# Kernel tuning notes

Hardware: AMD Instinct MI355X
Metric: run time of the kernel (lower is better)

## Reference

```python
import jax, jax.numpy as jnp
import numpy as np

N_NODES = 100000
N_EDGES = 1600000
IN_DIM, HID_DIM, OUT_DIM = 128, 128, 47
BN_EPS = 1e-5


def setup_inputs() -> dict:
    key = jax.random.key(0)
    ks = jax.random.split(key, 12)
    x = jax.random.normal(ks[0], (N_NODES, IN_DIM), dtype=jnp.float32)
    edge_index = jax.random.randint(ks[1], (2, N_EDGES), 0, N_NODES, dtype=jnp.int32)
    def glorot(k, fan_in, fan_out):
        s = jnp.sqrt(6.0 / (fan_in + fan_out))
        return jax.random.uniform(k, (fan_in, fan_out), jnp.float32, -s, s)
    return {
        "x": x,
        "edge_index": edge_index,
        "W0": glorot(ks[2], IN_DIM, HID_DIM), "b0": jnp.zeros((HID_DIM,), jnp.float32),
        "W1": glorot(ks[3], HID_DIM, HID_DIM), "b1": jnp.zeros((HID_DIM,), jnp.float32),
        "W2": glorot(ks[4], HID_DIM, OUT_DIM), "b2": jnp.zeros((OUT_DIM,), jnp.float32),
        "g0": jnp.ones((HID_DIM,), jnp.float32), "be0": jnp.zeros((HID_DIM,), jnp.float32),
        "g1": jnp.ones((HID_DIM,), jnp.float32), "be1": jnp.zeros((HID_DIM,), jnp.float32),
    }


def _gcn_norm(edge_index, n_nodes):
    # add self-loops, compute sym-normalized edge weights (PyG GCNConv default)
    loop = jnp.arange(n_nodes, dtype=edge_index.dtype)
    src = jnp.concatenate([edge_index[0], loop])
    dst = jnp.concatenate([edge_index[1], loop])
    deg = jax.ops.segment_sum(jnp.ones_like(dst, dtype=jnp.float32), dst,
                              num_segments=n_nodes)
    dinv = jnp.where(deg > 0, jax.lax.rsqrt(deg), 0.0)
    norm = dinv[src] * dinv[dst]  # [E + N]
    return src, dst, norm


def _conv(x, W, b, src, dst, norm, n_nodes):
    h = x @ W                                   # [N, d_out]
    msg = h[src] * norm[:, None]                # gather + scale
    out = jax.ops.segment_sum(msg, dst, num_segments=n_nodes)
    return out + b


def _batchnorm(h, gamma, beta):
    mean = jnp.mean(h, axis=0)
    var = jnp.mean(jnp.square(h - mean), axis=0)  # biased var (torch BN)
    return (h - mean) * jax.lax.rsqrt(var + BN_EPS) * gamma + beta


def reference(x, edge_index, W0, b0, W1, b1, W2, b2, g0, be0, g1, be1):
    n = x.shape[0]
    src, dst, norm = _gcn_norm(edge_index, n)
    h = _conv(x, W0, b0, src, dst, norm, n)
    h = jax.nn.relu(_batchnorm(h, g0, be0))     # dropout = identity (eval)
    h = _conv(h, W1, b1, src, dst, norm, n)
    h = jax.nn.relu(_batchnorm(h, g1, be1))
    h = _conv(h, W2, b2, src, dst, norm, n)
    return jax.nn.log_softmax(h, axis=-1)
```

## Files before the change

kernel.cpp:

```cpp
#include <hip/hip_runtime.h>
#include <math.h>

#define N_NODES 100000
#define N_EDGES 1600000
#define HID 128
#define OUTD 47
#define OSTR 48

#define NPB 128
#define NB 782
#define BCAP 2560
#define CHUNK 2048
#define NCHB 782
#define CWB 64

typedef short bf16x8 __attribute__((ext_vector_type(8)));
typedef float f32x4 __attribute__((ext_vector_type(4)));

__device__ inline unsigned short f2bf(float x) {
    union { float f; unsigned int u; } v; v.f = x;
    unsigned int r = v.u + 0x7fffu + ((v.u >> 16) & 1u);
    return (unsigned short)(r >> 16);
}
__device__ inline float bf_lo(unsigned int u) { return __uint_as_float(u << 16); }
__device__ inline float bf_hi(unsigned int u) { return __uint_as_float(u & 0xffff0000u); }

__device__ inline unsigned int src_chunk(unsigned int s) {
    return (s * 42950u) >> 28;
}


__global__ __launch_bounds__(256) void binA_k(
    const int* __restrict__ src, const int* __restrict__ dst,
    int* __restrict__ gcur, unsigned int* __restrict__ binned,
    const float* __restrict__ W0, const float* __restrict__ W1, const float* __restrict__ W2,
    unsigned short* __restrict__ Wt0, unsigned short* __restrict__ Wt1,
    unsigned short* __restrict__ Wt2)
{
    __shared__ unsigned int sortedL[CHUNK];
    __shared__ unsigned short bucketOf[CHUNK];
    __shared__ int cntL[NB];
    __shared__ int excL[NB];
    __shared__ int curL[NB];
    __shared__ int gposL[NB];
    __shared__ int partial[256];

    int t = threadIdx.x;

    if (blockIdx.x >= NCHB) {
        int i = (blockIdx.x - NCHB) * 256 + t;
        if (i < 16384) {
            int n = i >> 7, k = i & 127;
            Wt0[i] = f2bf(W0[k * 128 + n]);
            Wt1[i] = f2bf(W1[k * 128 + n]);
        }
        if (i < 48 * 128) {
            int n = i >> 7, k = i & 127;
            Wt2[i] = (n < OUTD) ? f2bf(W2[k * OUTD + n]) : (unsigned short)0;
        }
        return;
    }

    int e0 = blockIdx.x * CHUNK;

    for (int i = t; i < NB; i += 256) cntL[i] = 0;
    __syncthreads();

    for (int i = t; i < CHUNK; i += 256) {
        int e = e0 + i;
        if (e < N_EDGES) atomicAdd(&cntL[dst[e] >> 7], 1);
    }
    __syncthreads();

    int b4 = t * 4;
    int c0 = (b4 + 0 < NB) ? cntL[b4 + 0] : 0;
    int c1 = (b4 + 1 < NB) ? cntL[b4 + 1] : 0;
    int c2 = (b4 + 2 < NB) ? cntL[b4 + 2] : 0;
    int c3 = (b4 + 3 < NB) ? cntL[b4 + 3] : 0;
    int lsum = c0 + c1 + c2 + c3;
    partial[t] = lsum;
    __syncthreads();
    for (int off = 1; off < 256; off <<= 1) {
        int x = (t >= off) ? partial[t - off] : 0;
        __syncthreads();
        partial[t] += x;
        __syncthreads();
    }
    int pbase = partial[t] - lsum;
    if (b4 + 0 < NB) { excL[b4 + 0] = pbase;                curL[b4 + 0] = pbase; }
    if (b4 + 1 < NB) { excL[b4 + 1] = pbase + c0;           curL[b4 + 1] = pbase + c0; }
    if (b4 + 2 < NB) { excL[b4 + 2] = pbase + c0 + c1;      curL[b4 + 2] = pbase + c0 + c1; }
    if (b4 + 3 < NB) { excL[b4 + 3] = pbase + c0 + c1 + c2; curL[b4 + 3] = pbase + c0 + c1 + c2; }
    __syncthreads();

    int tot = partial[255];

    for (int i = t; i < CHUNK; i += 256) {
        int e = e0 + i;
        if (e < N_EDGES) {
            int d = dst[e];
            int s = src[e];
            int bkt = d >> 7;
            int pos = atomicAdd(&curL[bkt], 1);
            sortedL[pos] = ((unsigned int)s << 7) | (unsigned int)(d & 127);
            bucketOf[pos] = (unsigned short)bkt;
        }
    }
    __syncthreads();

    for (int b = t; b < NB; b += 256) {
        int c = cntL[b];
        gposL[b] = c ? atomicAdd(&gcur[b], c) : 0;
    }
    __syncthreads();

    for (int i = t; i < tot; i += 256) {
        unsigned int r = sortedL[i];
        int bkt = bucketOf[i];
        binned[(size_t)bkt * BCAP + gposL[bkt] + (i - excL[bkt])] = r;
    }
}


__global__ __launch_bounds__(256) void binB_k(
    const unsigned int* __restrict__ binned, const int* __restrict__ gcur,
    int2* __restrict__ rowse, float* __restrict__ dinv, int* __restrict__ colv)
{
    __shared__ unsigned int recL[BCAP];
    __shared__ int colL[BCAP];
    __shared__ int hist[2048];
    __shared__ int partial[256];

    int b = blockIdx.x, t = threadIdx.x;
    int cnt = gcur[b];
    int base = b * BCAP;
    const unsigned int* rp = binned + (size_t)b * BCAP;

    for (int i = t; i < 2048; i += 256) hist[i] = 0;
    __syncthreads();

    for (int i = t; i < cnt; i += 256) {
        unsigned int r = rp[i];
        recL[i] = r;
        unsigned int key = ((r & 127u) << 4) | src_chunk(r >> 7);
        atomicAdd(&hist[key], 1);
    }
    __syncthreads();

    int base8 = t * 8;
    int v[8], lsum = 0;
#pragma unroll
    for (int j = 0; j < 8; j++) { v[j] = hist[base8 + j]; lsum += v[j]; }
    partial[t] = lsum;
    __syncthreads();
    for (int off = 1; off < 256; off <<= 1) {
        int x = (t >= off) ? partial[t - off] : 0;
        __syncthreads();
        partial[t] += x;
        __syncthreads();
    }
    int run = partial[t] - lsum;
#pragma unroll
    for (int j = 0; j < 8; j++) { hist[base8 + j] = run; run += v[j]; }
    __syncthreads();

    if (t < NPB) {
        int node = b * NPB + t;
        if (node < N_NODES) {
            int start = hist[t << 4];
            int end = (t < NPB - 1) ? hist[(t + 1) << 4] : cnt;
            rowse[node] = make_int2(base + start, base + end);
            dinv[node] = rsqrtf((float)(end - start + 1));
        }
    }
    __syncthreads();

    for (int i = t; i < cnt; i += 256) {
        unsigned int r = recL[i];
        unsigned int key = ((r & 127u) << 4) | src_chunk(r >> 7);
        int pos = atomicAdd(&hist[key], 1);
        colL[pos] = (int)(r >> 7);
    }
    __syncthreads();
    for (int i = t; i < cnt; i += 256) colv[base + i] = colL[i];
}


template <int ABF16, int MODE, int NT, int OBF16>
__global__ __launch_bounds__(256) void gemm_k(
    const void* __restrict__ Ap, const unsigned short* __restrict__ Wt,
    const float* __restrict__ bnSum, const float* __restrict__ bnSq,
    const float* __restrict__ gam, const float* __restrict__ bet,
    const float* __restrict__ dinv, void* __restrict__ Outp,
    int ncols, int ostride)
{
    __shared__ unsigned short WtL[NT * 16][136];
    __shared__ float sS[128], sT[128];

    int t = threadIdx.x;
    if (MODE) {
        if (t < 128) {
            float mean = bnSum[t] * (1.0f / N_NODES);
            float var = bnSq[t] * (1.0f / N_NODES) - mean * mean;
            float inv = rsqrtf(var + 1e-5f);
            float s = gam[t] * inv;
            sS[t] = s;
            sT[t] = bet[t] - mean * s;
        }
    }

    const int TOT = NT * 16 * 128;
    for (int e = t * 8; e < TOT; e += 256 * 8) {
        int n = e >> 7, k = e & 127;
        uint4 v = *(const uint4*)(Wt + e);
        *(uint4*)&WtL[n][k] = v;
    }
    __syncthreads();

    int wave = t >> 6, lane = t & 63;
    int quad = lane >> 4, m16 = lane & 15;
    int rbase = blockIdx.x * 128 + wave * 32;

    f32x4 acc[2][NT];
#pragma unroll
    for (int rt = 0; rt < 2; rt++)
#pragma unroll
        for (int ct = 0; ct < NT; ct++) acc[rt][ct] = (f32x4){0.f, 0.f, 0.f, 0.f};

#pragma unroll
    for (int kc = 0; kc < 4; kc++) {
        int kb = kc * 32 + quad * 8;
        bf16x8 afrag[2];
#pragma unroll
        for (int rt = 0; rt < 2; rt++) {
            int row = rbase + rt * 16 + m16;
            bool rv = (row < N_NODES);
            if (ABF16) {
                uint4 v = make_uint4(0, 0, 0, 0);
                if (rv) v = *(const uint4*)((const unsigned short*)Ap + (size_t)row * 128 + kb);
                if (MODE) {
                    unsigned int uu[4] = {v.x, v.y, v.z, v.w};
                    unsigned short* fp = (unsigned short*)&afrag[rt];
#pragma unroll
                    for (int i = 0; i < 4; i++) {
                        int k0 = kb + 2 * i;
                        float lo = fmaxf(bf_lo(uu[i]) * sS[k0] + sT[k0], 0.f);
                        float hi = fmaxf(bf_hi(uu[i]) * sS[k0 + 1] + sT[k0 + 1], 0.f);
                        fp[2 * i] = f2bf(lo);
                        fp[2 * i + 1] = f2bf(hi);
                    }
                } else {
                    afrag[rt] = *(bf16x8*)&v;
                }
            } else {
                const float* ap = (const float*)Ap + (size_t)row * 128 + kb;
                float4 f0 = make_float4(0.f, 0.f, 0.f, 0.f), f1 = f0;
                if (rv) { f0 = *(const float4*)ap; f1 = *(const float4*)(ap + 4); }
                unsigned short* fp = (unsigned short*)&afrag[rt];
                fp[0] = f2bf(f0.x); fp[1] = f2bf(f0.y); fp[2] = f2bf(f0.z); fp[3] = f2bf(f0.w);
                fp[4] = f2bf(f1.x); fp[5] = f2bf(f1.y); fp[6] = f2bf(f1.z); fp[7] = f2bf(f1.w);
            }
        }
#pragma unroll
        for (int ct = 0; ct < NT; ct++) {
            bf16x8 bfrag = *(bf16x8*)&WtL[ct * 16 + m16][kb];
#pragma unroll
            for (int rt = 0; rt < 2; rt++)
                acc[rt][ct] = __builtin_amdgcn_mfma_f32_16x16x32_bf16(
                    afrag[rt], bfrag, acc[rt][ct], 0, 0, 0);
        }
    }

#pragma unroll
    for (int rt = 0; rt < 2; rt++)
#pragma unroll
        for (int r = 0; r < 4; r++) {
            int row = rbase + rt * 16 + quad * 4 + r;
            if (row < N_NODES) {
                float d = dinv[row];
#pragma unroll
                for (int ct = 0; ct < NT; ct++) {
                    int c = ct * 16 + m16;
                    if (c < ncols) {
                        float val = acc[rt][ct][r] * d;
                        if (OBF16)
                            ((unsigned short*)Outp)[(size_t)row * ostride + c] = f2bf(val);
                        else
                            ((float*)Outp)[(size_t)row * ostride + c] = val;
                    }
                }
            }
        }
}


__global__ __launch_bounds__(256) void agg_k(
    const unsigned int* __restrict__ H, const int2* __restrict__ rowse,
    const int* __restrict__ colv, const float* __restrict__ dinv,
    const float* __restrict__ bias, unsigned int* __restrict__ out)
{
    int gw = (blockIdx.x * 256 + threadIdx.x) >> 6;
    int lane = threadIdx.x & 63;
    if (gw >= N_NODES) return;
    int q = lane >> 4;
    int c = lane & 15;
    int2 se = rowse[gw];
    int rp = se.x, re = se.y;
    const uint4* H4 = (const uint4*)H;

    float a0 = 0.f, a1 = 0.f, a2 = 0.f, a3 = 0.f;
    float a4 = 0.f, a5 = 0.f, a6 = 0.f, a7 = 0.f;
    if (q == 0) {
        uint4 u = H4[(size_t)gw * 16 + c];
        a0 = bf_lo(u.x); a1 = bf_hi(u.x); a2 = bf_lo(u.y); a3 = bf_hi(u.y);
        a4 = bf_lo(u.z); a5 = bf_hi(u.z); a6 = bf_lo(u.w); a7 = bf_hi(u.w);
    }

    for (int j0 = rp; j0 < re; j0 += 64) {
        int idx = (j0 + lane < re) ? colv[j0 + lane] : 0;
        int n = min(64, re - j0);
        int nq = n >> 2;
        int t4 = 0;
        for (; t4 + 1 < nq; t4 += 2) {
            int sa = __shfl(idx, 4 * t4 + q);
            int sb = __shfl(idx, 4 * t4 + 4 + q);
            uint4 ua = H4[(size_t)sa * 16 + c];
            uint4 ub = H4[(size_t)sb * 16 + c];
            a0 += bf_lo(ua.x) + bf_lo(ub.x);
            a1 += bf_hi(ua.x) + bf_hi(ub.x);
            a2 += bf_lo(ua.y) + bf_lo(ub.y);
            a3 += bf_hi(ua.y) + bf_hi(ub.y);
            a4 += bf_lo(ua.z) + bf_lo(ub.z);
            a5 += bf_hi(ua.z) + bf_hi(ub.z);
            a6 += bf_lo(ua.w) + bf_lo(ub.w);
            a7 += bf_hi(ua.w) + bf_hi(ub.w);
        }
        if (t4 < nq) {
            int sa = __shfl(idx, 4 * t4 + q);
            uint4 ua = H4[(size_t)sa * 16 + c];
            a0 += bf_lo(ua.x); a1 += bf_hi(ua.x);
            a2 += bf_lo(ua.y); a3 += bf_hi(ua.y);
            a4 += bf_lo(ua.z); a5 += bf_hi(ua.z);
            a6 += bf_lo(ua.w); a7 += bf_hi(ua.w);
        }
        int rem = n & 3;
        if (rem) {
            int sa = __shfl(idx, (n - rem) + q);
            if (q < rem) {
                uint4 ua = H4[(size_t)sa * 16 + c];
                a0 += bf_lo(ua.x); a1 += bf_hi(ua.x);
                a2 += bf_lo(ua.y); a3 += bf_hi(ua.y);
                a4 += bf_lo(ua.z); a5 += bf_hi(ua.z);
                a6 += bf_lo(ua.w); a7 += bf_hi(ua.w);
            }
        }
    }

    a0 += __shfl_xor(a0, 16); a0 += __shfl_xor(a0, 32);
    a1 += __shfl_xor(a1, 16); a1 += __shfl_xor(a1, 32);
    a2 += __shfl_xor(a2, 16); a2 += __shfl_xor(a2, 32);
    a3 += __shfl_xor(a3, 16); a3 += __shfl_xor(a3, 32);
    a4 += __shfl_xor(a4, 16); a4 += __shfl_xor(a4, 32);
    a5 += __shfl_xor(a5, 16); a5 += __shfl_xor(a5, 32);
    a6 += __shfl_xor(a6, 16); a6 += __shfl_xor(a6, 32);
    a7 += __shfl_xor(a7, 16); a7 += __shfl_xor(a7, 32);

    if (q == 0) {
        float d = dinv[gw];
        float4 ba = ((const float4*)bias)[2 * c];
        float4 bb = ((const float4*)bias)[2 * c + 1];
        uint4 r;
        r.x = (unsigned int)f2bf(a0 * d + ba.x) | ((unsigned int)f2bf(a1 * d + ba.y) << 16);
        r.y = (unsigned int)f2bf(a2 * d + ba.z) | ((unsigned int)f2bf(a3 * d + ba.w) << 16);
        r.z = (unsigned int)f2bf(a4 * d + bb.x) | ((unsigned int)f2bf(a5 * d + bb.y) << 16);
        r.w = (unsigned int)f2bf(a6 * d + bb.z) | ((unsigned int)f2bf(a7 * d + bb.w) << 16);
        ((uint4*)out)[(size_t)gw * 16 + c] = r;
    }
}


__global__ __launch_bounds__(256) void agg_out_k(
    const unsigned int* __restrict__ H, const int2* __restrict__ rowse,
    const int* __restrict__ colv, const float* __restrict__ dinv,
    const float* __restrict__ b2, float* __restrict__ out)
{
    int gw = (blockIdx.x * 256 + threadIdx.x) >> 6;
    int lane = threadIdx.x & 63;
    if (gw >= N_NODES) return;
    int q = lane >> 4;
    int c = lane & 15;
    bool ld = c < 12;
    int2 se = rowse[gw];
    int rp = se.x, re = se.y;
    const uint2* H2 = (const uint2*)H;

    float a0 = 0.f, a1 = 0.f, a2 = 0.f, a3 = 0.f;
    if (q == 0 && ld) {
        uint2 u = H2[(size_t)gw * 12 + c];
        a0 = bf_lo(u.x); a1 = bf_hi(u.x); a2 = bf_lo(u.y); a3 = bf_hi(u.y);
    }

    for (int j0 = rp; j0 < re; j0 += 64) {
        int idx = (j0 + lane < re) ? colv[j0 + lane] : 0;
        int n = min(64, re - j0);
        int nq = n >> 2;
        int t4 = 0;
        for (; t4 + 1 < nq; t4 += 2) {
            int sa = __shfl(idx, 4 * t4 + q);
            int sb = __shfl(idx, 4 * t4 + 4 + q);
            if (ld) {
                uint2 ua = H2[(size_t)sa * 12 + c];
                uint2 ub = H2[(size_t)sb * 12 + c];
                a0 += bf_lo(ua.x) + bf_lo(ub.x);
                a1 += bf_hi(ua.x) + bf_hi(ub.x);
                a2 += bf_lo(ua.y) + bf_lo(ub.y);
                a3 += bf_hi(ua.y) + bf_hi(ub.y);
            }
        }
        if (t4 < nq) {
            int sa = __shfl(idx, 4 * t4 + q);
            if (ld) {
                uint2 ua = H2[(size_t)sa * 12 + c];
                a0 += bf_lo(ua.x); a1 += bf_hi(ua.x);
                a2 += bf_lo(ua.y); a3 += bf_hi(ua.y);
            }
        }
        int rem = n & 3;
        if (rem) {
            int sa = __shfl(idx, (n - rem) + q);
            if (q < rem && ld) {
                uint2 ua = H2[(size_t)sa * 12 + c];
                a0 += bf_lo(ua.x); a1 += bf_hi(ua.x);
                a2 += bf_lo(ua.y); a3 += bf_hi(ua.y);
            }
        }
    }

    a0 += __shfl_xor(a0, 16); a0 += __shfl_xor(a0, 32);
    a1 += __shfl_xor(a1, 16); a1 += __shfl_xor(a1, 32);
    a2 += __shfl_xor(a2, 16); a2 += __shfl_xor(a2, 32);
    a3 += __shfl_xor(a3, 16); a3 += __shfl_xor(a3, 32);

    float d = dinv[gw];
    int ch = c * 4;
    float v0 = -INFINITY, v1 = -INFINITY, v2 = -INFINITY, v3 = -INFINITY;
    if (ld) {
        v0 = a0 * d + b2[ch];
        v1 = a1 * d + b2[ch + 1];
        v2 = a2 * d + b2[ch + 2];
        if (ch + 3 < OUTD) v3 = a3 * d + b2[ch + 3];
    }
    float m = fmaxf(fmaxf(v0, v1), fmaxf(v2, v3));
    m = fmaxf(m, __shfl_xor(m, 1));
    m = fmaxf(m, __shfl_xor(m, 2));
    m = fmaxf(m, __shfl_xor(m, 4));
    m = fmaxf(m, __shfl_xor(m, 8));
    float e = 0.f;
    if (ld) {
        e = __expf(v0 - m) + __expf(v1 - m) + __expf(v2 - m);
        if (ch + 3 < OUTD) e += __expf(v3 - m);
    }
    float sum = e;
    sum += __shfl_xor(sum, 1);
    sum += __shfl_xor(sum, 2);
    sum += __shfl_xor(sum, 4);
    sum += __shfl_xor(sum, 8);
    float ls = logf(sum);
    if (q == 0 && ld) {
        float* op = out + (size_t)gw * OUTD + ch;
        op[0] = v0 - m - ls;
        op[1] = v1 - m - ls;
        op[2] = v2 - m - ls;
        if (ch + 3 < OUTD) op[3] = v3 - m - ls;
    }
}


__global__ __launch_bounds__(256) void bnstats_k(const unsigned int* __restrict__ H,
                                                 float* __restrict__ sum,
                                                 float* __restrict__ sq)
{
    __shared__ float2 ls[256], lq[256];
    int t = threadIdx.x;
    int idx = blockIdx.x * 256 + t;
    int stride = gridDim.x * 256;
    float sx = 0.f, sy = 0.f, qx = 0.f, qy = 0.f;
    for (; idx < N_NODES * 64; idx += stride) {
        unsigned int u = H[idx];
        float x = bf_lo(u), y = bf_hi(u);
        sx += x; sy += y; qx += x * x; qy += y * y;
    }
    ls[t] = make_float2(sx, sy);
    lq[t] = make_float2(qx, qy);
    __syncthreads();
    if (t < 64) {
        float2 a = ls[t], b = ls[t + 64], c = ls[t + 128], d = ls[t + 192];
        float2 e = lq[t], f = lq[t + 64], g = lq[t + 128], h = lq[t + 192];
        int c0 = t * 2;
        atomicAdd(&sum[c0],     a.x + b.x + c.x + d.x);
        atomicAdd(&sum[c0 + 1], a.y + b.y + c.y + d.y);
        atomicAdd(&sq[c0],      e.x + f.x + g.x + h.x);
        atomicAdd(&sq[c0 + 1],  e.y + f.y + g.y + h.y);
    }
}


extern "C" void kernel_launch(void* const* d_in, const int* in_sizes, int n_in,
                              void* d_out, int out_size, void* d_ws, size_t ws_size,
                              hipStream_t stream)
{
    const float* x   = (const float*)d_in[0];
    const int*   ei  = (const int*)d_in[1];
    const float* W0  = (const float*)d_in[2];
    const float* b0  = (const float*)d_in[3];
    const float* W1  = (const float*)d_in[4];
    const float* b1  = (const float*)d_in[5];
    const float* W2  = (const float*)d_in[6];
    const float* b2  = (const float*)d_in[7];
    const float* g0  = (const float*)d_in[8];
    const float* be0 = (const float*)d_in[9];
    const float* g1  = (const float*)d_in[10];
    const float* be1 = (const float*)d_in[11];
    const int* srcv = ei;
    const int* dstv = ei + N_EDGES;

    char* w = (char*)d_ws;
    unsigned int* H0 = (unsigned int*)w;  w += (size_t)N_NODES * 128 * 2;
    unsigned int* H1 = (unsigned int*)w;  w += (size_t)N_NODES * 128 * 2;
    unsigned int* Hf = (unsigned int*)w;  w += (size_t)N_NODES * OSTR * 2;
    unsigned int* binned = (unsigned int*)w; w += (size_t)NB * BCAP * 4;
    int* colv = (int*)w;        w += (size_t)NB * BCAP * 4;
    unsigned short* Wt0 = (unsigned short*)w; w += 16384 * 2;
    unsigned short* Wt1 = (unsigned short*)w; w += 16384 * 2;
    unsigned short* Wt2 = (unsigned short*)w; w += 48 * 128 * 2;
    int2* rowse = (int2*)w;     w += (size_t)N_NODES * 8;
    float* dinv = (float*)w;    w += (size_t)N_NODES * 4;
    int* gcur = (int*)w;        w += 784 * 4;
    float* bnS0 = (float*)w;    w += 128 * 4;
    float* bnQ0 = (float*)w;    w += 128 * 4;
    float* bnS1 = (float*)w;    w += 128 * 4;
    float* bnQ1 = (float*)w;    w += 128 * 4;

    int gb = (N_NODES + 127) / 128;
    int ab = (N_NODES * 64 + 255) / 256;

    hipMemsetAsync(gcur, 0, (784 + 512) * 4, stream);

    binA_k<<<NCHB + CWB, 256, 0, stream>>>(srcv, dstv, gcur, binned,
                                           W0, W1, W2, Wt0, Wt1, Wt2);
    binB_k<<<NB, 256, 0, stream>>>(binned, gcur, rowse, dinv, colv);

    gemm_k<0, 0, 8, 1><<<gb, 256, 0, stream>>>(x, Wt0, nullptr, nullptr, nullptr, nullptr,
                                               dinv, H0, 128, 128);
    agg_k<<<ab, 256, 0, stream>>>(H0, rowse, colv, dinv, b0, H1);
    bnstats_k<<<512, 256, 0, stream>>>(H1, bnS0, bnQ0);

    gemm_k<1, 1, 8, 1><<<gb, 256, 0, stream>>>(H1, Wt1, bnS0, bnQ0, g0, be0,
                                               dinv, H0, 128, 128);
    agg_k<<<ab, 256, 0, stream>>>(H0, rowse, colv, dinv, b1, H1);
    bnstats_k<<<512, 256, 0, stream>>>(H1, bnS1, bnQ1);

    gemm_k<1, 1, 3, 1><<<gb, 256, 0, stream>>>(H1, Wt2, bnS1, bnQ1, g1, be1,
                                               dinv, Hf, OUTD, OSTR);
    agg_out_k<<<ab, 256, 0, stream>>>(Hf, rowse, colv, dinv, b2, (float*)d_out);
}
```

Before: 474.6 us.

## Fuse batchnorm statistics into aggregation and process four nodes per wavefront

The aggregation kernel now gives each 16-lane quarter of a wavefront its own destination node, instead of splitting one node's edges across the whole wavefront and reducing with cross-lane shuffles. Each quarter loads up to 16 neighbour indices at a time and issues up to eight gathers before accumulating. The separate bnstats kernel is removed: per-channel sum and sum-of-squares are reduced in shared memory across a 1024-thread block and added atomically. This drops two launches and one full re-read of the hidden activations. In exchange, nodes with different degrees in one wavefront cause lane divergence, and statistics are taken from pre-rounding fp32 values rather than the stored bf16 ones.

```diff
diff --git a/kernel.cpp b/kernel.cpp
--- a/kernel.cpp
+++ b/kernel.cpp
@@ -13,6 +13,7 @@
 #define CHUNK 2048
 #define NCHB 782
 #define CWB 64
+#define NAB 1563
 
 typedef short bf16x8 __attribute__((ext_vector_type(8)));
 typedef float f32x4 __attribute__((ext_vector_type(4)));
@@ -294,87 +295,145 @@
 }
 
 
-__global__ __launch_bounds__(256) void agg_k(
+__global__ __launch_bounds__(1024) void agg4_k(
     const unsigned int* __restrict__ H, const int2* __restrict__ rowse,
     const int* __restrict__ colv, const float* __restrict__ dinv,
-    const float* __restrict__ bias, unsigned int* __restrict__ out)
+    const float* __restrict__ bias,
+    float* __restrict__ bnSum, float* __restrict__ bnSq,
+    unsigned int* __restrict__ out)
 {
-    int gw = (blockIdx.x * 256 + threadIdx.x) >> 6;
-    int lane = threadIdx.x & 63;
-    if (gw >= N_NODES) return;
-    int q = lane >> 4;
-    int c = lane & 15;
-    int2 se = rowse[gw];
-    int rp = se.x, re = se.y;
+    __shared__ float red[2][16][16][8];
+
+    int t = threadIdx.x;
+    int w = t >> 6, lane = t & 63;
+    int q = lane >> 4, c = lane & 15;
+    int qb = q << 4;
+    int node = blockIdx.x * 64 + w * 4 + q;
+    bool valid = node < N_NODES;
+
     const uint4* H4 = (const uint4*)H;
 
     float a0 = 0.f, a1 = 0.f, a2 = 0.f, a3 = 0.f;
     float a4 = 0.f, a5 = 0.f, a6 = 0.f, a7 = 0.f;
-    if (q == 0) {
-        uint4 u = H4[(size_t)gw * 16 + c];
+    int rp = 0, re = 0;
+    float dv = 0.f;
+    if (valid) {
+        int2 se = rowse[node];
+        rp = se.x; re = se.y;
+        dv = dinv[node];
+        uint4 u = H4[(size_t)node * 16 + c];
         a0 = bf_lo(u.x); a1 = bf_hi(u.x); a2 = bf_lo(u.y); a3 = bf_hi(u.y);
         a4 = bf_lo(u.z); a5 = bf_hi(u.z); a6 = bf_lo(u.w); a7 = bf_hi(u.w);
     }
 
-    for (int j0 = rp; j0 < re; j0 += 64) {
-        int idx = (j0 + lane < re) ? colv[j0 + lane] : 0;
-        int n = min(64, re - j0);
-        int nq = n >> 2;
-        int t4 = 0;
-        for (; t4 + 1 < nq; t4 += 2) {
-            int sa = __shfl(idx, 4 * t4 + q);
-            int sb = __shfl(idx, 4 * t4 + 4 + q);
-            uint4 ua = H4[(size_t)sa * 16 + c];
-            uint4 ub = H4[(size_t)sb * 16 + c];
-            a0 += bf_lo(ua.x) + bf_lo(ub.x);
-            a1 += bf_hi(ua.x) + bf_hi(ub.x);
-            a2 += bf_lo(ua.y) + bf_lo(ub.y);
-            a3 += bf_hi(ua.y) + bf_hi(ub.y);
-            a4 += bf_lo(ua.z) + bf_lo(ub.z);
-            a5 += bf_hi(ua.z) + bf_hi(ub.z);
-            a6 += bf_lo(ua.w) + bf_lo(ub.w);
-            a7 += bf_hi(ua.w) + bf_hi(ub.w);
-        }
-        if (t4 < nq) {
-            int sa = __shfl(idx, 4 * t4 + q);
-            uint4 ua = H4[(size_t)sa * 16 + c];
-            a0 += bf_lo(ua.x); a1 += bf_hi(ua.x);
-            a2 += bf_lo(ua.y); a3 += bf_hi(ua.y);
-            a4 += bf_lo(ua.z); a5 += bf_hi(ua.z);
-            a6 += bf_lo(ua.w); a7 += bf_hi(ua.w);
-        }
-        int rem = n & 3;
-        if (rem) {
-            int sa = __shfl(idx, (n - rem) + q);
-            if (q < rem) {
-                uint4 ua = H4[(size_t)sa * 16 + c];
-                a0 += bf_lo(ua.x); a1 += bf_hi(ua.x);
-                a2 += bf_lo(ua.y); a3 += bf_hi(ua.y);
-                a4 += bf_lo(ua.z); a5 += bf_hi(ua.z);
-                a6 += bf_lo(ua.w); a7 += bf_hi(ua.w);
-            }
-        }
-    }
-
-    a0 += __shfl_xor(a0, 16); a0 += __shfl_xor(a0, 32);
-    a1 += __shfl_xor(a1, 16); a1 += __shfl_xor(a1, 32);
-    a2 += __shfl_xor(a2, 16); a2 += __shfl_xor(a2, 32);
-    a3 += __shfl_xor(a3, 16); a3 += __shfl_xor(a3, 32);
-    a4 += __shfl_xor(a4, 16); a4 += __shfl_xor(a4, 32);
-    a5 += __shfl_xor(a5, 16); a5 += __shfl_xor(a5, 32);
-    a6 += __shfl_xor(a6, 16); a6 += __shfl_xor(a6, 32);
-    a7 += __shfl_xor(a7, 16); a7 += __shfl_xor(a7, 32);
-
+    for (int j0 = rp; j0 < re; j0 += 16) {
+        int m = min(16, re - j0);
+        int idx = (c < m) ? colv[j0 + c] : 0;
+        int tt = 0;
+        for (; tt + 8 <= m; tt += 8) {
+            int s0 = __shfl(idx, qb + tt + 0);
+            int s1 = __shfl(idx, qb + tt + 1);
+            int s2 = __shfl(idx, qb + tt + 2);
+            int s3 = __shfl(idx, qb + tt + 3);
+            int s4 = __shfl(idx, qb + tt + 4);
+            int s5 = __shfl(idx, qb + tt + 5);
+            int s6 = __shfl(idx, qb + tt + 6);
+            int s7 = __shfl(idx, qb + tt + 7);
+            uint4 u0 = H4[(size_t)s0 * 16 + c];
+            uint4 u1 = H4[(size_t)s1 * 16 + c];
+            uint4 u2 = H4[(size_t)s2 * 16 + c];
+            uint4 u3 = H4[(size_t)s3 * 16 + c];
+            uint4 u4 = H4[(size_t)s4 * 16 + c];
+            uint4 u5 = H4[(size_t)s5 * 16 + c];
+            uint4 u6 = H4[(size_t)s6 * 16 + c];
+            uint4 u7 = H4[(size_t)s7 * 16 + c];
+            a0 += (bf_lo(u0.x) + bf_lo(u1.x)) + (bf_lo(u2.x) + bf_lo(u3.x))
+                + (bf_lo(u4.x) + bf_lo(u5.x)) + (bf_lo(u6.x) + bf_lo(u7.x));
+            a1 += (bf_hi(u0.x) + bf_hi(u1.x)) + (bf_hi(u2.x) + bf_hi(u3.x))
+                + (bf_hi(u4.x) + bf_hi(u5.x)) + (bf_hi(u6.x) + bf_hi(u7.x));
+            a2 += (bf_lo(u0.y) + bf_lo(u1.y)) + (bf_lo(u2.y) + bf_lo(u3.y))
+                + (bf_lo(u4.y) + bf_lo(u5.y)) + (bf_lo(u6.y) + bf_lo(u7.y));
+            a3 += (bf_hi(u0.y) + bf_hi(u1.y)) + (bf_hi(u2.y) + bf_hi(u3.y))
+                + (bf_hi(u4.y) + bf_hi(u5.y)) + (bf_hi(u6.y) + bf_hi(u7.y));
+            a4 += (bf_lo(u0.z) + bf_lo(u1.z)) + (bf_lo(u2.z) + bf_lo(u3.z))
+                + (bf_lo(u4.z) + bf_lo(u5.z)) + (bf_lo(u6.z) + bf_lo(u7.z));
+            a5 += (bf_hi(u0.z) + bf_hi(u1.z)) + (bf_hi(u2.z) + bf_hi(u3.z))
+                + (bf_hi(u4.z) + bf_hi(u5.z)) + (bf_hi(u6.z) + bf_hi(u7.z));
+            a6 += (bf_lo(u0.w) + bf_lo(u1.w)) + (bf_lo(u2.w) + bf_lo(u3.w))
+                + (bf_lo(u4.w) + bf_lo(u5.w)) + (bf_lo(u6.w) + bf_lo(u7.w));
+            a7 += (bf_hi(u0.w) + bf_hi(u1.w)) + (bf_hi(u2.w) + bf_hi(u3.w))
+                + (bf_hi(u4.w) + bf_hi(u5.w)) + (bf_hi(u6.w) + bf_hi(u7.w));
+        }
+        for (; tt + 4 <= m; tt += 4) {
+            int s0 = __shfl(idx, qb + tt + 0);
+            int s1 = __shfl(idx, qb + tt + 1);
+            int s2 = __shfl(idx, qb + tt + 2);
+            int s3 = __shfl(idx, qb + tt + 3);
+            uint4 u0 = H4[(size_t)s0 * 16 + c];
+            uint4 u1 = H4[(size_t)s1 * 16 + c];
+            uint4 u2 = H4[(size_t)s2 * 16 + c];
+            uint4 u3 = H4[(size_t)s3 * 16 + c];
+            a0 += (bf_lo(u0.x) + bf_lo(u1.x)) + (bf_lo(u2.x) + bf_lo(u3.x));
+            a1 += (bf_hi(u0.x) + bf_hi(u1.x)) + (bf_hi(u2.x) + bf_hi(u3.x));
+            a2 += (bf_lo(u0.y) + bf_lo(u1.y)) + (bf_lo(u2.y) + bf_lo(u3.y));
+            a3 += (bf_hi(u0.y) + bf_hi(u1.y)) + (bf_hi(u2.y) + bf_hi(u3.y));
+            a4 += (bf_lo(u0.z) + bf_lo(u1.z)) + (bf_lo(u2.z) + bf_lo(u3.z));
+            a5 += (bf_hi(u0.z) + bf_hi(u1.z)) + (bf_hi(u2.z) + bf_hi(u3.z));
+            a6 += (bf_lo(u0.w) + bf_lo(u1.w)) + (bf_lo(u2.w) + bf_lo(u3.w));
+            a7 += (bf_hi(u0.w) + bf_hi(u1.w)) + (bf_hi(u2.w) + bf_hi(u3.w));
+        }
+        for (; tt < m; tt++) {
+            int s0 = __shfl(idx, qb + tt);
+            uint4 u0 = H4[(size_t)s0 * 16 + c];
+            a0 += bf_lo(u0.x); a1 += bf_hi(u0.x);
+            a2 += bf_lo(u0.y); a3 += bf_hi(u0.y);
+            a4 += bf_lo(u0.z); a5 += bf_hi(u0.z);
+            a6 += bf_lo(u0.w); a7 += bf_hi(u0.w);
+        }
+    }
+
+    float4 ba = ((const float4*)bias)[2 * c];
+    float4 bb = ((const float4*)bias)[2 * c + 1];
+    float v0 = a0 * dv + ba.x, v1 = a1 * dv + ba.y;
+    float v2 = a2 * dv + ba.z, v3 = a3 * dv + ba.w;
+    float v4 = a4 * dv + bb.x, v5 = a5 * dv + bb.y;
+    float v6 = a6 * dv + bb.z, v7 = a7 * dv + bb.w;
+    if (valid) {
+        uint4 r;
+        r.x = (unsigned int)f2bf(v0) | ((unsigned int)f2bf(v1) << 16);
+        r.y = (unsigned int)f2bf(v2) | ((unsigned int)f2bf(v3) << 16);
+        r.z = (unsigned int)f2bf(v4) | ((unsigned int)f2bf(v5) << 16);
+        r.w = (unsigned int)f2bf(v6) | ((unsigned int)f2bf(v7) << 16);
+        ((uint4*)out)[(size_t)node * 16 + c] = r;
+    }
+
+    float sv[8], qv[8];
+    float vv[8] = {v0, v1, v2, v3, v4, v5, v6, v7};
+#pragma unroll
+    for (int k = 0; k < 8; k++) {
+        float x = valid ? vv[k] : 0.f;
+        sv[k] = x; qv[k] = x * x;
+    }
+#pragma unroll
+    for (int k = 0; k < 8; k++) {
+        sv[k] += __shfl_xor(sv[k], 16); sv[k] += __shfl_xor(sv[k], 32);
+        qv[k] += __shfl_xor(qv[k], 16); qv[k] += __shfl_xor(qv[k], 32);
+    }
     if (q == 0) {
-        float d = dinv[gw];
-        float4 ba = ((const float4*)bias)[2 * c];
-        float4 bb = ((const float4*)bias)[2 * c + 1];
-        uint4 r;
-        r.x = (unsigned int)f2bf(a0 * d + ba.x) | ((unsigned int)f2bf(a1 * d + ba.y) << 16);
-        r.y = (unsigned int)f2bf(a2 * d + ba.z) | ((unsigned int)f2bf(a3 * d + ba.w) << 16);
-        r.z = (unsigned int)f2bf(a4 * d + bb.x) | ((unsigned int)f2bf(a5 * d + bb.y) << 16);
-        r.w = (unsigned int)f2bf(a6 * d + bb.z) | ((unsigned int)f2bf(a7 * d + bb.w) << 16);
-        ((uint4*)out)[(size_t)gw * 16 + c] = r;
+#pragma unroll
+        for (int k = 0; k < 8; k++) {
+            red[0][w][c][k] = sv[k];
+            red[1][w][c][k] = qv[k];
+        }
+    }
+    __syncthreads();
+    if (t < 256) {
+        int part = t >> 7, ch = t & 127;
+        int cc = ch >> 3, k = ch & 7;
+        float tot = 0.f;
+#pragma unroll
+        for (int ww = 0; ww < 16; ww++) tot += red[part][ww][cc][k];
+        atomicAdd((part ? bnSq : bnSum) + ch, tot);
     }
 }
 
@@ -472,35 +531,6 @@
         op[1] = v1 - m - ls;
         op[2] = v2 - m - ls;
         if (ch + 3 < OUTD) op[3] = v3 - m - ls;
-    }
-}
-
-
-__global__ __launch_bounds__(256) void bnstats_k(const unsigned int* __restrict__ H,
-                                                 float* __restrict__ sum,
-                                                 float* __restrict__ sq)
-{
-    __shared__ float2 ls[256], lq[256];
-    int t = threadIdx.x;
-    int idx = blockIdx.x * 256 + t;
-    int stride = gridDim.x * 256;
-    float sx = 0.f, sy = 0.f, qx = 0.f, qy = 0.f;
-    for (; idx < N_NODES * 64; idx += stride) {
-        unsigned int u = H[idx];
-        float x = bf_lo(u), y = bf_hi(u);
-        sx += x; sy += y; qx += x * x; qy += y * y;
-    }
-    ls[t] = make_float2(sx, sy);
-    lq[t] = make_float2(qx, qy);
-    __syncthreads();
-    if (t < 64) {
-        float2 a = ls[t], b = ls[t + 64], c = ls[t + 128], d = ls[t + 192];
-        float2 e = lq[t], f = lq[t + 64], g = lq[t + 128], h = lq[t + 192];
-        int c0 = t * 2;
-        atomicAdd(&sum[c0],     a.x + b.x + c.x + d.x);
-        atomicAdd(&sum[c0 + 1], a.y + b.y + c.y + d.y);
-        atomicAdd(&sq[c0],      e.x + f.x + g.x + h.x);
-        atomicAdd(&sq[c0 + 1],  e.y + f.y + g.y + h.y);
     }
 }
 
@@ -552,13 +582,11 @@
 
     gemm_k<0, 0, 8, 1><<<gb, 256, 0, stream>>>(x, Wt0, nullptr, nullptr, nullptr, nullptr,
                                                dinv, H0, 128, 128);
-    agg_k<<<ab, 256, 0, stream>>>(H0, rowse, colv, dinv, b0, H1);
-    bnstats_k<<<512, 256, 0, stream>>>(H1, bnS0, bnQ0);
+    agg4_k<<<NAB, 1024, 0, stream>>>(H0, rowse, colv, dinv, b0, bnS0, bnQ0, H1);
 
     gemm_k<1, 1, 8, 1><<<gb, 256, 0, stream>>>(H1, Wt1, bnS0, bnQ0, g0, be0,
                                                dinv, H0, 128, 128);
-    agg_k<<<ab, 256, 0, stream>>>(H0, rowse, colv, dinv, b1, H1);
-    bnstats_k<<<512, 256, 0, stream>>>(H1, bnS1, bnQ1);
+    agg4_k<<<NAB, 1024, 0, stream>>>(H0, rowse, colv, dinv, b1, bnS1, bnQ1, H1);
 
     gemm_k<1, 1, 3, 1><<<gb, 256, 0, stream>>>(H1, Wt2, bnS1, bnQ1, g1, be1,
                                                dinv, Hf, OUTD, OSTR);
```

Result: faster. 453.3 us (-4.5%).

## Fuse batchnorm statistics into aggregation and prefetch GEMM A rows with packed bf16 converts

Applied to the files above, without the earlier changes.

The batchnorm sum and sum-of-squares are now accumulated inside the aggregation kernel's epilogue into 64 striped partial slots per channel, and the separate bnstats pass that reread H1 is removed. The GEMM sums the 64 partial slots when it builds the scale and shift. The GEMM also loads all of its A fragments up front, which allows more loads in flight, and uses the hardware v_cvt_pk_bf16_f32 instruction in place of software rounding. The cost is one extra atomic per channel per block, a larger memset, and more registers held in the GEMM. The early return for out-of-range waves was dropped before the syncthreads, and the row count divides exactly into blocks here.

```diff
diff --git a/kernel.cpp b/kernel.cpp
--- a/kernel.cpp
+++ b/kernel.cpp
@@ -24,6 +24,12 @@
 }
 __device__ inline float bf_lo(unsigned int u) { return __uint_as_float(u << 16); }
 __device__ inline float bf_hi(unsigned int u) { return __uint_as_float(u & 0xffff0000u); }
+
+__device__ inline unsigned int cvt_pk_bf16(float lo, float hi) {
+    unsigned int r;
+    asm("v_cvt_pk_bf16_f32 %0, %1, %2" : "=v"(r) : "v"(lo), "v"(hi));
+    return r;
+}
 
 __device__ inline unsigned int src_chunk(unsigned int s) {
     return (s * 42950u) >> 28;
@@ -195,17 +201,21 @@
     int ncols, int ostride)
 {
     __shared__ unsigned short WtL[NT * 16][136];
-    __shared__ float sS[128], sT[128];
+    __shared__ float2 sST[128];
 
     int t = threadIdx.x;
     if (MODE) {
         if (t < 128) {
-            float mean = bnSum[t] * (1.0f / N_NODES);
-            float var = bnSq[t] * (1.0f / N_NODES) - mean * mean;
+            float s_ = 0.f, q_ = 0.f;
+            for (int sl = 0; sl < 64; sl++) {
+                s_ += bnSum[sl * 128 + t];
+                q_ += bnSq[sl * 128 + t];
+            }
+            float mean = s_ * (1.0f / N_NODES);
+            float var = q_ * (1.0f / N_NODES) - mean * mean;
             float inv = rsqrtf(var + 1e-5f);
             float s = gam[t] * inv;
-            sS[t] = s;
-            sT[t] = bet[t] - mean * s;
+            sST[t] = make_float2(s, bet[t] - mean * s);
         }
     }
 
@@ -221,6 +231,36 @@
     int quad = lane >> 4, m16 = lane & 15;
     int rbase = blockIdx.x * 128 + wave * 32;
 
+    uint4 av[2][4];
+#pragma unroll
+    for (int rt = 0; rt < 2; rt++) {
+        int row = rbase + rt * 16 + m16;
+        bool rv = (row < N_NODES);
+        if (ABF16) {
+            const uint4* ap = (const uint4*)((const unsigned short*)Ap + (size_t)row * 128);
+#pragma unroll
+            for (int kc = 0; kc < 4; kc++)
+                av[rt][kc] = rv ? ap[kc * 4 + quad] : make_uint4(0, 0, 0, 0);
+        } else {
+            const float4* ap = (const float4*)((const float*)Ap + (size_t)row * 128);
+            float4 f[8];
+#pragma unroll
+            for (int kc = 0; kc < 4; kc++) {
+                f[2 * kc]     = rv ? ap[kc * 8 + quad * 2]     : make_float4(0.f, 0.f, 0.f, 0.f);
+                f[2 * kc + 1] = rv ? ap[kc * 8 + quad * 2 + 1] : make_float4(0.f, 0.f, 0.f, 0.f);
+            }
+#pragma unroll
+            for (int kc = 0; kc < 4; kc++) {
+                uint4 v;
+                v.x = cvt_pk_bf16(f[2 * kc].x, f[2 * kc].y);
+                v.y = cvt_pk_bf16(f[2 * kc].z, f[2 * kc].w);
+                v.z = cvt_pk_bf16(f[2 * kc + 1].x, f[2 * kc + 1].y);
+                v.w = cvt_pk_bf16(f[2 * kc + 1].z, f[2 * kc + 1].w);
+                av[rt][kc] = v;
+            }
+        }
+    }
+
     f32x4 acc[2][NT];
 #pragma unroll
     for (int rt = 0; rt < 2; rt++)
@@ -233,32 +273,19 @@
         bf16x8 afrag[2];
 #pragma unroll
         for (int rt = 0; rt < 2; rt++) {
-            int row = rbase + rt * 16 + m16;
-            bool rv = (row < N_NODES);
-            if (ABF16) {
-                uint4 v = make_uint4(0, 0, 0, 0);
-                if (rv) v = *(const uint4*)((const unsigned short*)Ap + (size_t)row * 128 + kb);
-                if (MODE) {
-                    unsigned int uu[4] = {v.x, v.y, v.z, v.w};
-                    unsigned short* fp = (unsigned short*)&afrag[rt];
-#pragma unroll
-                    for (int i = 0; i < 4; i++) {
-                        int k0 = kb + 2 * i;
-                        float lo = fmaxf(bf_lo(uu[i]) * sS[k0] + sT[k0], 0.f);
-                        float hi = fmaxf(bf_hi(uu[i]) * sS[k0 + 1] + sT[k0 + 1], 0.f);
-                        fp[2 * i] = f2bf(lo);
-                        fp[2 * i + 1] = f2bf(hi);
-                    }
-                } else {
-                    afrag[rt] = *(bf16x8*)&v;
+            if (MODE) {
+                unsigned int uu[4] = {av[rt][kc].x, av[rt][kc].y, av[rt][kc].z, av[rt][kc].w};
+                unsigned int* up = (unsigned int*)&afrag[rt];
+#pragma unroll
+                for (int i = 0; i < 4; i++) {
+                    int k0 = kb + 2 * i;
+                    float2 sa = sST[k0], sb = sST[k0 + 1];
+                    float lo = fmaxf(bf_lo(uu[i]) * sa.x + sa.y, 0.f);
+                    float hi = fmaxf(bf_hi(uu[i]) * sb.x + sb.y, 0.f);
+                    up[i] = cvt_pk_bf16(lo, hi);
                 }
             } else {
-                const float* ap = (const float*)Ap + (size_t)row * 128 + kb;
-                float4 f0 = make_float4(0.f, 0.f, 0.f, 0.f), f1 = f0;
-                if (rv) { f0 = *(const float4*)ap; f1 = *(const float4*)(ap + 4); }
-                unsigned short* fp = (unsigned short*)&afrag[rt];
-                fp[0] = f2bf(f0.x); fp[1] = f2bf(f0.y); fp[2] = f2bf(f0.z); fp[3] = f2bf(f0.w);
-                fp[4] = f2bf(f1.x); fp[5] = f2bf(f1.y); fp[6] = f2bf(f1.z); fp[7] = f2bf(f1.w);
+                afrag[rt] = *(bf16x8*)&av[rt][kc];
             }
         }
 #pragma unroll
@@ -284,7 +311,8 @@
                     if (c < ncols) {
                         float val = acc[rt][ct][r] * d;
                         if (OBF16)
-                            ((unsigned short*)Outp)[(size_t)row * ostride + c] = f2bf(val);
+                            ((unsigned short*)Outp)[(size_t)row * ostride + c] =
+                                (unsigned short)cvt_pk_bf16(val, 0.f);
                         else
                             ((float*)Outp)[(size_t)row * ostride + c] = val;
                     }
@@ -297,11 +325,16 @@
 __global__ __launch_bounds__(256) void agg_k(
     const unsigned int* __restrict__ H, const int2* __restrict__ rowse,
     const int* __restrict__ colv, const float* __restrict__ dinv,
-    const float* __restrict__ bias, unsigned int* __restrict__ out)
+    const float* __restrict__ bias,
+    float* __restrict__ bnPS, float* __restrict__ bnPQ,
+    unsigned int* __restrict__ out)
 {
-    int gw = (blockIdx.x * 256 + threadIdx.x) >> 6;
-    int lane = threadIdx.x & 63;
-    if (gw >= N_NODES) return;
+    __shared__ float red[2][4][16][8];
+
+    int t = threadIdx.x;
+    int gw = (blockIdx.x * 256 + t) >> 6;
+    int lane = t & 63;
+    int w = t >> 6;
     int q = lane >> 4;
     int c = lane & 15;
     int2 se = rowse[gw];
@@ -369,12 +402,32 @@
         float d = dinv[gw];
         float4 ba = ((const float4*)bias)[2 * c];
         float4 bb = ((const float4*)bias)[2 * c + 1];
+        float vv[8];
+        vv[0] = a0 * d + ba.x; vv[1] = a1 * d + ba.y;
+        vv[2] = a2 * d + ba.z; vv[3] = a3 * d + ba.w;
+        vv[4] = a4 * d + bb.x; vv[5] = a5 * d + bb.y;
+        vv[6] = a6 * d + bb.z; vv[7] = a7 * d + bb.w;
         uint4 r;
-        r.x = (unsigned int)f2bf(a0 * d + ba.x) | ((unsigned int)f2bf(a1 * d + ba.y) << 16);
-        r.y = (unsigned int)f2bf(a2 * d + ba.z) | ((unsigned int)f2bf(a3 * d + ba.w) << 16);
-        r.z = (unsigned int)f2bf(a4 * d + bb.x) | ((unsigned int)f2bf(a5 * d + bb.y) << 16);
-        r.w = (unsigned int)f2bf(a6 * d + bb.z) | ((unsigned int)f2bf(a7 * d + bb.w) << 16);
+        r.x = cvt_pk_bf16(vv[0], vv[1]);
+        r.y = cvt_pk_bf16(vv[2], vv[3]);
+        r.z = cvt_pk_bf16(vv[4], vv[5]);
+        r.w = cvt_pk_bf16(vv[6], vv[7]);
         ((uint4*)out)[(size_t)gw * 16 + c] = r;
+#pragma unroll
+        for (int k = 0; k < 8; k++) {
+            red[0][w][c][k] = vv[k];
+            red[1][w][c][k] = vv[k] * vv[k];
+        }
+    }
+    __syncthreads();
+
+    {
+        int part = t >> 7;
+        int ch = t & 127;
+        int cc = ch >> 3, k = ch & 7;
+        float s = red[part][0][cc][k] + red[part][1][cc][k]
+                + red[part][2][cc][k] + red[part][3][cc][k];
+        atomicAdd((part ? bnPQ : bnPS) + (blockIdx.x & 63) * 128 + ch, s);
     }
 }
 
@@ -472,35 +525,6 @@
         op[1] = v1 - m - ls;
         op[2] = v2 - m - ls;
         if (ch + 3 < OUTD) op[3] = v3 - m - ls;
-    }
-}
-
-
-__global__ __launch_bounds__(256) void bnstats_k(const unsigned int* __restrict__ H,
-                                                 float* __restrict__ sum,
-                                                 float* __restrict__ sq)
-{
-    __shared__ float2 ls[256], lq[256];
-    int t = threadIdx.x;
-    int idx = blockIdx.x * 256 + t;
-    int stride = gridDim.x * 256;
-    float sx = 0.f, sy = 0.f, qx = 0.f, qy = 0.f;
-    for (; idx < N_NODES * 64; idx += stride) {
-        unsigned int u = H[idx];
-        float x = bf_lo(u), y = bf_hi(u);
-        sx += x; sy += y; qx += x * x; qy += y * y;
-    }
-    ls[t] = make_float2(sx, sy);
-    lq[t] = make_float2(qx, qy);
-    __syncthreads();
-    if (t < 64) {
-        float2 a = ls[t], b = ls[t + 64], c = ls[t + 128], d = ls[t + 192];
-        float2 e = lq[t], f = lq[t + 64], g = lq[t + 128], h = lq[t + 192];
-        int c0 = t * 2;
-        atomicAdd(&sum[c0],     a.x + b.x + c.x + d.x);
-        atomicAdd(&sum[c0 + 1], a.y + b.y + c.y + d.y);
-        atomicAdd(&sq[c0],      e.x + f.x + g.x + h.x);
-        atomicAdd(&sq[c0 + 1],  e.y + f.y + g.y + h.y);
     }
 }
 
@@ -536,15 +560,15 @@
     int2* rowse = (int2*)w;     w += (size_t)N_NODES * 8;
     float* dinv = (float*)w;    w += (size_t)N_NODES * 4;
     int* gcur = (int*)w;        w += 784 * 4;
-    float* bnS0 = (float*)w;    w += 128 * 4;
-    float* bnQ0 = (float*)w;    w += 128 * 4;
-    float* bnS1 = (float*)w;    w += 128 * 4;
-    float* bnQ1 = (float*)w;    w += 128 * 4;
+    float* bnP0S = (float*)w;   w += 64 * 128 * 4;
+    float* bnP0Q = (float*)w;   w += 64 * 128 * 4;
+    float* bnP1S = (float*)w;   w += 64 * 128 * 4;
+    float* bnP1Q = (float*)w;   w += 64 * 128 * 4;
 
     int gb = (N_NODES + 127) / 128;
     int ab = (N_NODES * 64 + 255) / 256;
 
-    hipMemsetAsync(gcur, 0, (784 + 512) * 4, stream);
+    hipMemsetAsync(gcur, 0, 784 * 4 + 4 * 64 * 128 * 4, stream);
 
     binA_k<<<NCHB + CWB, 256, 0, stream>>>(srcv, dstv, gcur, binned,
                                            W0, W1, W2, Wt0, Wt1, Wt2);
@@ -552,15 +576,13 @@
 
     gemm_k<0, 0, 8, 1><<<gb, 256, 0, stream>>>(x, Wt0, nullptr, nullptr, nullptr, nullptr,
                                                dinv, H0, 128, 128);
-    agg_k<<<ab, 256, 0, stream>>>(H0, rowse, colv, dinv, b0, H1);
-    bnstats_k<<<512, 256, 0, stream>>>(H1, bnS0, bnQ0);
-
-    gemm_k<1, 1, 8, 1><<<gb, 256, 0, stream>>>(H1, Wt1, bnS0, bnQ0, g0, be0,
+    agg_k<<<ab, 256, 0, stream>>>(H0, rowse, colv, dinv, b0, bnP0S, bnP0Q, H1);
+
+    gemm_k<1, 1, 8, 1><<<gb, 256, 0, stream>>>(H1, Wt1, bnP0S, bnP0Q, g0, be0,
                                                dinv, H0, 128, 128);
-    agg_k<<<ab, 256, 0, stream>>>(H0, rowse, colv, dinv, b1, H1);
-    bnstats_k<<<512, 256, 0, stream>>>(H1, bnS1, bnQ1);
-
-    gemm_k<1, 1, 3, 1><<<gb, 256, 0, stream>>>(H1, Wt2, bnS1, bnQ1, g1, be1,
+    agg_k<<<ab, 256, 0, stream>>>(H0, rowse, colv, dinv, b1, bnP1S, bnP1Q, H1);
+
+    gemm_k<1, 1, 3, 1><<<gb, 256, 0, stream>>>(H1, Wt2, bnP1S, bnP1Q, g1, be1,
                                                dinv, Hf, OUTD, OSTR);
     agg_out_k<<<ab, 256, 0, stream>>>(Hf, rowse, colv, dinv, b2, (float*)d_out);
 }
```

Result: faster. 411.1 us (-13.4%).
